# Optimization experiments

Hardware: AMD Instinct MI355X
Metric: run time of the kernel (lower is better)

Reference implementation:

```python
import jax, jax.numpy as jnp
import numpy as np

D_MODEL = 1024
N_HEADS = 16
H_DIM = D_MODEL // N_HEADS
B, T = 2, 2048


def setup_inputs() -> dict:
    key = jax.random.key(0)
    ks = jax.random.split(key, 11)
    s = 1.0 / np.sqrt(D_MODEL)
    inp = {
        "q": jax.random.normal(ks[0], (B, T, D_MODEL), dtype=jnp.float32),
        "k": jax.random.normal(ks[1], (B, T, D_MODEL), dtype=jnp.float32),
        "v": jax.random.normal(ks[2], (B, T, D_MODEL), dtype=jnp.float32),
        "Wq": jax.random.normal(ks[3], (D_MODEL, D_MODEL), dtype=jnp.float32) * s,
        "bq": jnp.zeros((D_MODEL,), dtype=jnp.float32),
        "Wk": jax.random.normal(ks[4], (D_MODEL, D_MODEL), dtype=jnp.float32) * s,
        "bk": jnp.zeros((D_MODEL,), dtype=jnp.float32),
        "Wv": jax.random.normal(ks[5], (D_MODEL, D_MODEL), dtype=jnp.float32) * s,
        "bv": jnp.zeros((D_MODEL,), dtype=jnp.float32),
        "Wo": jax.random.normal(ks[6], (D_MODEL, D_MODEL), dtype=jnp.float32) * s,
        "bo": jnp.zeros((D_MODEL,), dtype=jnp.float32),
    }
    return inp


def reference(q, k, v, Wq, bq, Wk, bk, Wv, bv, Wo, bo):
    # Linear projections (W stored so that y = x @ W + b)
    qp = q @ Wq + bq  # [B,T,D]
    kp = k @ Wk + bk
    vp = v @ Wv + bv
    Bz, Tz, _ = qp.shape
    # [B,T,H,h] -> [B,H,T,h]
    qh = qp.reshape(Bz, Tz, N_HEADS, H_DIM).transpose(0, 2, 1, 3)
    kh = kp.reshape(Bz, Tz, N_HEADS, H_DIM).transpose(0, 2, 1, 3)
    vh = vp.reshape(Bz, Tz, N_HEADS, H_DIM).transpose(0, 2, 1, 3)
    scale = 1.0 / np.sqrt(H_DIM).astype(np.float32)
    scores = jnp.einsum('bhqd,bhkd->bhqk', qh, kh) * scale  # [B,H,T,T]
    attn = jax.nn.softmax(scores, axis=-1)  # dropout is identity in eval
    ctx = jnp.einsum('bhqk,bhkd->bhqd', attn, vh)  # [B,H,T,h]
    ctx = ctx.transpose(0, 2, 1, 3).reshape(Bz, Tz, D_MODEL)
    return ctx @ Wo + bo
```

## Files before the change

### kernel.cpp

```cpp
#include <hip/hip_runtime.h>

typedef __bf16 bf16x8 __attribute__((ext_vector_type(8)));
typedef float f32x4 __attribute__((ext_vector_type(4)));
typedef float f32x16 __attribute__((ext_vector_type(16)));
typedef unsigned short u16;
typedef unsigned short u16x8 __attribute__((ext_vector_type(8)));
typedef unsigned int u32;

#define MROWS 4096
#define DMODEL 1024
#define TSEQ 2048

__device__ __forceinline__ u32 bfr(float x) {
    u32 u = __float_as_uint(x);
    return (u + 0x7FFFu + ((u >> 16) & 1u)) >> 16;
}
__device__ __forceinline__ u32 pk2(float lo, float hi) { return bfr(lo) | (bfr(hi) << 16); }

__device__ __forceinline__ u32 cvtpk(float lo, float hi) {
    u32 r;
    asm("v_cvt_pk_bf16_f32 %0, %1, %2" : "=v"(r) : "v"(lo), "v"(hi));
    return r;
}

__device__ __forceinline__ void gl_lds16(const void* g, void* l) {
    __builtin_amdgcn_global_load_lds(
        (const __attribute__((address_space(1))) unsigned int*)g,
        (__attribute__((address_space(3))) unsigned int*)l, 16, 0, 0);
}

__global__ __launch_bounds__(256) void cvt_x(const float* __restrict__ q,
                                             const float* __restrict__ k,
                                             const float* __restrict__ v,
                                             u16* __restrict__ X) {
    int z = blockIdx.y;
    const float* src = (z == 0) ? q : (z == 1) ? k : v;
    size_t idx = ((size_t)blockIdx.x * 256 + threadIdx.x) * 8;
    const float4* s4 = (const float4*)(src + idx);
    float4 a = s4[0], b = s4[1];
    uint4 r;
    r.x = pk2(a.x, a.y); r.y = pk2(a.z, a.w);
    r.z = pk2(b.x, b.y); r.w = pk2(b.z, b.w);
    *(uint4*)(X + (size_t)z * 4194304 + idx) = r;
}

__global__ __launch_bounds__(256) void cvt_w(const float* __restrict__ w0,
                                             const float* __restrict__ w1,
                                             const float* __restrict__ w2,
                                             const float* __restrict__ w3,
                                             u16* __restrict__ Wt) {
    int z = blockIdx.z;
    const float* W = (z == 0) ? w0 : (z == 1) ? w1 : (z == 2) ? w2 : w3;
    u16* dst = Wt + (size_t)z * 1048576;
    __shared__ float tile[32][33];
    int n0 = blockIdx.x * 32, k0 = blockIdx.y * 32;
    int tx = threadIdx.x & 31, ty = threadIdx.x >> 5;
#pragma unroll
    for (int r = 0; r < 4; r++) {
        int row = ty + r * 8;
        tile[row][tx] = W[(size_t)(k0 + row) * DMODEL + n0 + tx];
    }
    __syncthreads();
#pragma unroll
    for (int r = 0; r < 4; r++) {
        int row = ty + r * 8;
        dst[(size_t)(n0 + row) * DMODEL + k0 + tx] = (u16)bfr(tile[tx][row]);
    }
}

template <int OUT_BF16>
__global__ __launch_bounds__(256) void gemm_bt(const u16* __restrict__ Abase,
                                               const u16* __restrict__ Btbase,
                                               const float* __restrict__ b0,
                                               const float* __restrict__ b1,
                                               const float* __restrict__ b2,
                                               void* __restrict__ Cout, int ldc) {
    int z = blockIdx.z;
    const u16* A  = Abase + (size_t)z * MROWS * DMODEL;
    const u16* Bt = Btbase + (size_t)z * DMODEL * DMODEL;
    const float* bias = (z == 0) ? b0 : (z == 1) ? b1 : b2;
    int id = blockIdx.y * 8 + blockIdx.x;
    int swz = (id & 7) * 32 + (id >> 3);
    int brow = (swz >> 3) * 128, bcol = (swz & 7) * 128;
    int t = threadIdx.x, lane = t & 63, wid = t >> 6;
    int wr = wid >> 1, wc = wid & 1;
    int lrow = lane & 15, g = lane >> 4;

    __shared__ __align__(16) u16 Asm[2][128 * 32];
    __shared__ __align__(16) u16 Bsm[2][128 * 32];

    f32x4 zero4 = {0.f, 0.f, 0.f, 0.f};
    f32x4 acc[4][4];
#pragma unroll
    for (int i = 0; i < 4; i++)
#pragma unroll
        for (int j = 0; j < 4; j++) acc[i][j] = zero4;

    auto stage = [&](int buf, int kt) {
        int k0 = kt * 32;
#pragma unroll
        for (int i = 0; i < 2; i++) {
            int c = i * 256 + wid * 64 + lane;
            int row = c >> 2, kc = c & 3;
            gl_lds16(A + (size_t)(brow + row) * DMODEL + k0 + kc * 8,
                     &Asm[buf][(i * 256 + wid * 64) * 8]);
            gl_lds16(Bt + (size_t)(bcol + row) * DMODEL + k0 + kc * 8,
                     &Bsm[buf][(i * 256 + wid * 64) * 8]);
        }
    };

    stage(0, 0);
    __syncthreads();
    for (int kt = 0; kt < 32; ++kt) {
        int cur = kt & 1;
        if (kt < 31) stage(cur ^ 1, kt + 1);
        bf16x8 af[4], bfv[4];
#pragma unroll
        for (int mi = 0; mi < 4; mi++)
            af[mi] = *(const bf16x8*)&Asm[cur][(wr * 64 + mi * 16 + lrow) * 32 + g * 8];
#pragma unroll
        for (int nj = 0; nj < 4; nj++)
            bfv[nj] = *(const bf16x8*)&Bsm[cur][(wc * 64 + nj * 16 + lrow) * 32 + g * 8];
#pragma unroll
        for (int mi = 0; mi < 4; mi++)
#pragma unroll
            for (int nj = 0; nj < 4; nj++)
                acc[mi][nj] = __builtin_amdgcn_mfma_f32_16x16x32_bf16(af[mi], bfv[nj], acc[mi][nj], 0, 0, 0);
        __syncthreads();
    }
#pragma unroll
    for (int nj = 0; nj < 4; nj++) {
        int n = bcol + wc * 64 + nj * 16 + lrow;
        float bv = bias[n];
#pragma unroll
        for (int mi = 0; mi < 4; mi++) {
#pragma unroll
            for (int r = 0; r < 4; r++) {
                int row = brow + wr * 64 + mi * 16 + g * 4 + r;
                float val = acc[mi][nj][r] + bv;
                if (OUT_BF16)
                    ((u16*)Cout)[(size_t)row * ldc + z * DMODEL + n] = (u16)bfr(val);
                else
                    ((float*)Cout)[(size_t)row * ldc + n] = val;
            }
        }
    }
}

__global__ __launch_bounds__(512, 1) void attn(const u16* __restrict__ QKV, u16* __restrict__ CTX) {
    int id = blockIdx.y * 8 + blockIdx.x;
    int swz = (id & 7) * 32 + (id >> 3);
    int qt = swz & 7;
    int bh = swz >> 3;
    int head = bh & 15;
    size_t base = (size_t)(bh >> 4) * TSEQ * 3072;
    int t = threadIdx.x;
    int tl = t & 255;
    int grp = t >> 8;
    int lane = t & 63, wid = t >> 6;
    int lw = wid & 3;
    int l31 = lane & 31, hf = lane >> 5;

    __shared__ __align__(16) u16 SH[32768];
    u16* Kg = SH + grp * 16384;
    u16* Vg = SH + grp * 16384 + 8192;

    int qwave = qt * 256 + lw * 64;
    const u16* QpA = QKV + base + (size_t)(qwave + l31) * 3072 + head * 64;
    const u16* QpB = QpA + 32 * 3072;
    bf16x8 qfA[4], qfB[4];
#pragma unroll
    for (int c = 0; c < 4; c++) {
        qfA[c] = *(const bf16x8*)(QpA + c * 16 + hf * 8);
        qfB[c] = *(const bf16x8*)(QpB + c * 16 + hf * 8);
    }

    f32x16 oA0 = {}, oA1 = {}, oB0 = {}, oB1 = {};
    float lA = 0.f, lB = 0.f;
    const float mC = 0.18033688f;

    int vkv = (tl & 31) * 2;
    int vd0 = (tl >> 5) * 8;
    int vslot = (vkv & ~12) | ((vkv & 4) << 1) | ((vkv & 8) >> 1);
    u16x8 vr0, vr1;

    auto stageK = [&](int buf, int kvb) {
#pragma unroll
        for (int i = 0; i < 2; i++) {
            int c = i * 256 + lw * 64 + lane;
            int kv = c >> 3, kc = (c & 7) ^ (kv & 7);
            gl_lds16(QKV + base + (size_t)(kvb * 64 + kv) * 3072 + 1024 + head * 64 + kc * 8,
                     &Kg[buf * 4096 + (i * 256 + lw * 64) * 8]);
        }
    };
    auto loadV = [&](int kvb) {
        const u16* Vp = QKV + base + (size_t)(kvb * 64) * 3072 + 2048 + head * 64;
        vr0 = *(const u16x8*)(Vp + (size_t)vkv * 3072 + vd0);
        vr1 = *(const u16x8*)(Vp + (size_t)(vkv + 1) * 3072 + vd0);
    };
    auto writeV = [&](int buf) {
#pragma unroll
        for (int e = 0; e < 8; e++) {
            int d = vd0 + e;
            int kvs = vslot ^ ((d >> 4) << 4) ^ ((d & 7) << 3);
            u32 p = (u32)vr0[e] | ((u32)vr1[e] << 16);
            *(u32*)&Vg[buf * 4096 + d * 64 + kvs] = p;
        }
    };

    int kvb0 = grp * 16;
    stageK(0, kvb0);
    loadV(kvb0);
    writeV(0);
    __syncthreads();

    int kx = (l31 & 7) * 8;

    for (int j = 0; j < 16; ++j) {
        int cur = j & 1, nxt = cur ^ 1;
        if (j < 15) { stageK(nxt, kvb0 + j + 1); loadV(kvb0 + j + 1); }

        f32x16 s0A = {}, s1A = {}, s0B = {}, s1B = {};
        const u16* kr0 = &Kg[cur * 4096 + l31 * 64];
        const u16* kr1 = kr0 + 32 * 64;
        __builtin_amdgcn_s_setprio(1);
#pragma unroll
        for (int c = 0; c < 4; c++) {
            int slot = ((2 * c + hf) * 8) ^ kx;
            bf16x8 a0 = *(const bf16x8*)(kr0 + slot);
            bf16x8 a1 = *(const bf16x8*)(kr1 + slot);
            s0A = __builtin_amdgcn_mfma_f32_32x32x16_bf16(a0, qfA[c], s0A, 0, 0, 0);
            s1A = __builtin_amdgcn_mfma_f32_32x32x16_bf16(a1, qfA[c], s1A, 0, 0, 0);
            s0B = __builtin_amdgcn_mfma_f32_32x32x16_bf16(a0, qfB[c], s0B, 0, 0, 0);
            s1B = __builtin_amdgcn_mfma_f32_32x32x16_bf16(a1, qfB[c], s1B, 0, 0, 0);
        }
        __builtin_amdgcn_s_setprio(0);

        float p0A[16], p1A[16], p0B[16], p1B[16];
#pragma unroll
        for (int r = 0; r < 16; r++) {
            p0A[r] = __builtin_amdgcn_exp2f(s0A[r] * mC);
            p1A[r] = __builtin_amdgcn_exp2f(s1A[r] * mC);
            p0B[r] = __builtin_amdgcn_exp2f(s0B[r] * mC);
            p1B[r] = __builtin_amdgcn_exp2f(s1B[r] * mC);
        }
        float sa = 0.f, sb = 0.f, sc = 0.f, sd = 0.f;
#pragma unroll
        for (int r = 0; r < 8; r++) {
            sa += p0A[r] + p0A[r + 8];
            sb += p1A[r] + p1A[r + 8];
            sc += p0B[r] + p0B[r + 8];
            sd += p1B[r] + p1B[r + 8];
        }
        lA += sa + sb;
        lB += sc + sd;

        union FragU { u32 u[4]; bf16x8 v; };
        bf16x8 paA[4], paB[4];
        {
            FragU fA, fB2, fC, fD;
#pragma unroll
            for (int w = 0; w < 4; w++) {
                fA.u[w]  = cvtpk(p0A[2 * w],     p0A[2 * w + 1]);
                fB2.u[w] = cvtpk(p0A[8 + 2 * w], p0A[9 + 2 * w]);
                fC.u[w]  = cvtpk(p1A[2 * w],     p1A[2 * w + 1]);
                fD.u[w]  = cvtpk(p1A[8 + 2 * w], p1A[9 + 2 * w]);
            }
            paA[0] = fA.v; paA[1] = fB2.v; paA[2] = fC.v; paA[3] = fD.v;
#pragma unroll
            for (int w = 0; w < 4; w++) {
                fA.u[w]  = cvtpk(p0B[2 * w],     p0B[2 * w + 1]);
                fB2.u[w] = cvtpk(p0B[8 + 2 * w], p0B[9 + 2 * w]);
                fC.u[w]  = cvtpk(p1B[2 * w],     p1B[2 * w + 1]);
                fD.u[w]  = cvtpk(p1B[8 + 2 * w], p1B[9 + 2 * w]);
            }
            paB[0] = fA.v; paB[1] = fB2.v; paB[2] = fC.v; paB[3] = fD.v;
        }

        if (j < 15) writeV(nxt);

        __builtin_amdgcn_s_setprio(1);
#pragma unroll
        for (int kc = 0; kc < 4; kc++) {
            int d0 = l31;
            int sl0 = ((2 * kc + hf) ^ (d0 & 7) ^ ((d0 >> 4) << 1)) * 8;
            bf16x8 v0 = *(const bf16x8*)&Vg[cur * 4096 + d0 * 64 + sl0];
            int d1 = 32 + l31;
            int sl1 = ((2 * kc + hf) ^ (d1 & 7) ^ ((d1 >> 4) << 1)) * 8;
            bf16x8 v1 = *(const bf16x8*)&Vg[cur * 4096 + d1 * 64 + sl1];
            oA0 = __builtin_amdgcn_mfma_f32_32x32x16_bf16(paA[kc], v0, oA0, 0, 0, 0);
            oA1 = __builtin_amdgcn_mfma_f32_32x32x16_bf16(paA[kc], v1, oA1, 0, 0, 0);
            oB0 = __builtin_amdgcn_mfma_f32_32x32x16_bf16(paB[kc], v0, oB0, 0, 0, 0);
            oB1 = __builtin_amdgcn_mfma_f32_32x32x16_bf16(paB[kc], v1, oB1, 0, 0, 0);
        }
        __builtin_amdgcn_s_setprio(0);
        __syncthreads();
    }

    lA += __shfl_xor(lA, 32);
    lB += __shfl_xor(lB, 32);

    float* FB = (float*)SH;
    if (grp == 1) {
#pragma unroll
        for (int r = 0; r < 16; r++) {
            FB[lw * 2048 + r * 64 + lane]        = oA0[r];
            FB[lw * 2048 + 1024 + r * 64 + lane] = oA1[r];
        }
        FB[8192 + lw * 64 + lane] = lA;
    }
    __syncthreads();
    if (grp == 0) {
        float l1 = FB[8192 + lw * 64 + lane];
        float rl = 1.0f / (lA + l1);
#pragma unroll
        for (int r = 0; r < 16; r++) {
            int qr = (r & 3) + 8 * (r >> 2) + 4 * hf;
            float rr = __shfl(rl, qr);
            float po0 = FB[lw * 2048 + r * 64 + lane];
            float po1 = FB[lw * 2048 + 1024 + r * 64 + lane];
            size_t rowoff = ((size_t)(bh >> 4) * TSEQ + qwave + qr) * DMODEL + head * 64;
            CTX[rowoff + l31]      = (u16)bfr((oA0[r] + po0) * rr);
            CTX[rowoff + 32 + l31] = (u16)bfr((oA1[r] + po1) * rr);
        }
    }
    __syncthreads();
    if (grp == 1) {
#pragma unroll
        for (int r = 0; r < 16; r++) {
            FB[lw * 2048 + r * 64 + lane]        = oB0[r];
            FB[lw * 2048 + 1024 + r * 64 + lane] = oB1[r];
        }
        FB[8192 + lw * 64 + lane] = lB;
    }
    __syncthreads();
    if (grp == 0) {
        float l1 = FB[8192 + lw * 64 + lane];
        float rl = 1.0f / (lB + l1);
#pragma unroll
        for (int r = 0; r < 16; r++) {
            int qr = (r & 3) + 8 * (r >> 2) + 4 * hf;
            float rr = __shfl(rl, qr);
            float po0 = FB[lw * 2048 + r * 64 + lane];
            float po1 = FB[lw * 2048 + 1024 + r * 64 + lane];
            size_t rowoff = ((size_t)(bh >> 4) * TSEQ + qwave + 32 + qr) * DMODEL + head * 64;
            CTX[rowoff + l31]      = (u16)bfr((oB0[r] + po0) * rr);
            CTX[rowoff + 32 + l31] = (u16)bfr((oB1[r] + po1) * rr);
        }
    }
}

extern "C" void kernel_launch(void* const* d_in, const int* in_sizes, int n_in,
                              void* d_out, int out_size, void* d_ws, size_t ws_size,
                              hipStream_t stream) {
    const float* q  = (const float*)d_in[0];
    const float* k  = (const float*)d_in[1];
    const float* v  = (const float*)d_in[2];
    const float* Wq = (const float*)d_in[3];
    const float* bq = (const float*)d_in[4];
    const float* Wk = (const float*)d_in[5];
    const float* bk = (const float*)d_in[6];
    const float* Wv = (const float*)d_in[7];
    const float* bv = (const float*)d_in[8];
    const float* Wo = (const float*)d_in[9];
    const float* bo = (const float*)d_in[10];

    char* ws = (char*)d_ws;
    u16* Xbf = (u16*)ws;
    u16* Wt  = (u16*)(ws + 25165824);
    u16* QKV = (u16*)(ws + 25165824 + 8388608);
    u16* CTX = Xbf;

    cvt_x<<<dim3(2048, 3), 256, 0, stream>>>(q, k, v, Xbf);
    cvt_w<<<dim3(32, 32, 4), 256, 0, stream>>>(Wq, Wk, Wv, Wo, Wt);
    gemm_bt<1><<<dim3(8, 32, 3), 256, 0, stream>>>(Xbf, Wt, bq, bk, bv, QKV, 3072);
    attn<<<dim3(8, 32), 512, 0, stream>>>(QKV, CTX);
    gemm_bt<0><<<dim3(8, 32, 1), 256, 0, stream>>>(CTX, Wt + 3 * 1048576, bo, bo, bo, d_out, 1024);
}
```

Measured before the change: 125.7 us.

## Fuse fp32-to-bf16 input conversion into QKV GEMM and split attention KV four ways

Drops the separate cvt_x kernel: the QKV projection GEMM now reads fp32 activations directly into registers, converts them to bf16 with v_cvt_pk_bf16_f32 and writes them to LDS. This removes one kernel launch and a full bf16 round trip of the activations through HBM, but A loads are now register-staged rather than direct-to-LDS. Separately, the attention kernel moves to 1024 threads with four KV-split groups of 8 blocks each, single-buffered K/V and an extra barrier per iteration. Partial outputs are combined across four groups through LDS in four phases, which raises parallelism but adds synchronization and reduction cost.

```diff
diff --git a/kernel.cpp b/kernel.cpp
--- a/kernel.cpp
+++ b/kernel.cpp
@@ -15,7 +15,6 @@
     u32 u = __float_as_uint(x);
     return (u + 0x7FFFu + ((u >> 16) & 1u)) >> 16;
 }
-__device__ __forceinline__ u32 pk2(float lo, float hi) { return bfr(lo) | (bfr(hi) << 16); }
 
 __device__ __forceinline__ u32 cvtpk(float lo, float hi) {
     u32 r;
@@ -27,21 +26,6 @@
     __builtin_amdgcn_global_load_lds(
         (const __attribute__((address_space(1))) unsigned int*)g,
         (__attribute__((address_space(3))) unsigned int*)l, 16, 0, 0);
-}
-
-__global__ __launch_bounds__(256) void cvt_x(const float* __restrict__ q,
-                                             const float* __restrict__ k,
-                                             const float* __restrict__ v,
-                                             u16* __restrict__ X) {
-    int z = blockIdx.y;
-    const float* src = (z == 0) ? q : (z == 1) ? k : v;
-    size_t idx = ((size_t)blockIdx.x * 256 + threadIdx.x) * 8;
-    const float4* s4 = (const float4*)(src + idx);
-    float4 a = s4[0], b = s4[1];
-    uint4 r;
-    r.x = pk2(a.x, a.y); r.y = pk2(a.z, a.w);
-    r.z = pk2(b.x, b.y); r.w = pk2(b.z, b.w);
-    *(uint4*)(X + (size_t)z * 4194304 + idx) = r;
 }
 
 __global__ __launch_bounds__(256) void cvt_w(const float* __restrict__ w0,
@@ -68,15 +52,17 @@
     }
 }
 
-template <int OUT_BF16>
-__global__ __launch_bounds__(256) void gemm_bt(const u16* __restrict__ Abase,
+template <int A_F32, int OUT_BF16>
+__global__ __launch_bounds__(256) void gemm_bt(const void* __restrict__ a0,
+                                               const void* __restrict__ a1,
+                                               const void* __restrict__ a2,
                                                const u16* __restrict__ Btbase,
                                                const float* __restrict__ b0,
                                                const float* __restrict__ b1,
                                                const float* __restrict__ b2,
                                                void* __restrict__ Cout, int ldc) {
     int z = blockIdx.z;
-    const u16* A  = Abase + (size_t)z * MROWS * DMODEL;
+    const void* Az = (z == 0) ? a0 : (z == 1) ? a1 : a2;
     const u16* Bt = Btbase + (size_t)z * DMODEL * DMODEL;
     const float* bias = (z == 0) ? b0 : (z == 1) ? b1 : b2;
     int id = blockIdx.y * 8 + blockIdx.x;
@@ -96,24 +82,63 @@
 #pragma unroll
         for (int j = 0; j < 4; j++) acc[i][j] = zero4;
 
-    auto stage = [&](int buf, int kt) {
+    float4 ar[2][2];
+
+    auto issueA = [&](int kt) {
         int k0 = kt * 32;
 #pragma unroll
         for (int i = 0; i < 2; i++) {
             int c = i * 256 + wid * 64 + lane;
             int row = c >> 2, kc = c & 3;
-            gl_lds16(A + (size_t)(brow + row) * DMODEL + k0 + kc * 8,
+            const float* ap = (const float*)Az + (size_t)(brow + row) * DMODEL + k0 + kc * 8;
+            ar[i][0] = *(const float4*)ap;
+            ar[i][1] = *(const float4*)(ap + 4);
+        }
+    };
+    auto writeA = [&](int buf) {
+#pragma unroll
+        for (int i = 0; i < 2; i++) {
+            int c = i * 256 + wid * 64 + lane;
+            uint4 w;
+            w.x = cvtpk(ar[i][0].x, ar[i][0].y);
+            w.y = cvtpk(ar[i][0].z, ar[i][0].w);
+            w.z = cvtpk(ar[i][1].x, ar[i][1].y);
+            w.w = cvtpk(ar[i][1].z, ar[i][1].w);
+            *(uint4*)&Asm[buf][c * 8] = w;
+        }
+    };
+    auto stageA16 = [&](int buf, int kt) {
+        int k0 = kt * 32;
+#pragma unroll
+        for (int i = 0; i < 2; i++) {
+            int c = i * 256 + wid * 64 + lane;
+            int row = c >> 2, kc = c & 3;
+            gl_lds16((const u16*)Az + (size_t)(brow + row) * DMODEL + k0 + kc * 8,
                      &Asm[buf][(i * 256 + wid * 64) * 8]);
+        }
+    };
+    auto stageB = [&](int buf, int kt) {
+        int k0 = kt * 32;
+#pragma unroll
+        for (int i = 0; i < 2; i++) {
+            int c = i * 256 + wid * 64 + lane;
+            int row = c >> 2, kc = c & 3;
             gl_lds16(Bt + (size_t)(bcol + row) * DMODEL + k0 + kc * 8,
                      &Bsm[buf][(i * 256 + wid * 64) * 8]);
         }
     };
 
-    stage(0, 0);
-    __syncthreads();
+    if constexpr (A_F32) { issueA(0); stageB(0, 0); writeA(0); }
+    else                 { stageA16(0, 0); stageB(0, 0); }
+    __syncthreads();
+
     for (int kt = 0; kt < 32; ++kt) {
-        int cur = kt & 1;
-        if (kt < 31) stage(cur ^ 1, kt + 1);
+        int cur = kt & 1, nxt = cur ^ 1;
+        if (kt < 31) {
+            if constexpr (A_F32) issueA(kt + 1);
+            else                 stageA16(nxt, kt + 1);
+            stageB(nxt, kt + 1);
+        }
         bf16x8 af[4], bfv[4];
 #pragma unroll
         for (int mi = 0; mi < 4; mi++)
@@ -126,6 +151,7 @@
 #pragma unroll
             for (int nj = 0; nj < 4; nj++)
                 acc[mi][nj] = __builtin_amdgcn_mfma_f32_16x16x32_bf16(af[mi], bfv[nj], acc[mi][nj], 0, 0, 0);
+        if constexpr (A_F32) { if (kt < 31) writeA(nxt); }
         __syncthreads();
     }
 #pragma unroll
@@ -147,7 +173,7 @@
     }
 }
 
-__global__ __launch_bounds__(512, 1) void attn(const u16* __restrict__ QKV, u16* __restrict__ CTX) {
+__global__ __launch_bounds__(1024, 1) void attn(const u16* __restrict__ QKV, u16* __restrict__ CTX) {
     int id = blockIdx.y * 8 + blockIdx.x;
     int swz = (id & 7) * 32 + (id >> 3);
     int qt = swz & 7;
@@ -157,13 +183,13 @@
     int t = threadIdx.x;
     int tl = t & 255;
     int grp = t >> 8;
-    int lane = t & 63, wid = t >> 6;
-    int lw = wid & 3;
+    int lane = t & 63;
+    int lw = (t >> 6) & 3;
     int l31 = lane & 31, hf = lane >> 5;
 
     __shared__ __align__(16) u16 SH[32768];
-    u16* Kg = SH + grp * 16384;
-    u16* Vg = SH + grp * 16384 + 8192;
+    u16* Kl = SH + grp * 8192;
+    u16* Vl = SH + grp * 8192 + 4096;
 
     int qwave = qt * 256 + lw * 64;
     const u16* QpA = QKV + base + (size_t)(qwave + l31) * 3072 + head * 64;
@@ -184,13 +210,13 @@
     int vslot = (vkv & ~12) | ((vkv & 4) << 1) | ((vkv & 8) >> 1);
     u16x8 vr0, vr1;
 
-    auto stageK = [&](int buf, int kvb) {
+    auto stageK = [&](int kvb) {
 #pragma unroll
         for (int i = 0; i < 2; i++) {
             int c = i * 256 + lw * 64 + lane;
             int kv = c >> 3, kc = (c & 7) ^ (kv & 7);
             gl_lds16(QKV + base + (size_t)(kvb * 64 + kv) * 3072 + 1024 + head * 64 + kc * 8,
-                     &Kg[buf * 4096 + (i * 256 + lw * 64) * 8]);
+                     &Kl[(i * 256 + lw * 64) * 8]);
         }
     };
     auto loadV = [&](int kvb) {
@@ -198,30 +224,28 @@
         vr0 = *(const u16x8*)(Vp + (size_t)vkv * 3072 + vd0);
         vr1 = *(const u16x8*)(Vp + (size_t)(vkv + 1) * 3072 + vd0);
     };
-    auto writeV = [&](int buf) {
+    auto writeV = [&]() {
 #pragma unroll
         for (int e = 0; e < 8; e++) {
             int d = vd0 + e;
             int kvs = vslot ^ ((d >> 4) << 4) ^ ((d & 7) << 3);
             u32 p = (u32)vr0[e] | ((u32)vr1[e] << 16);
-            *(u32*)&Vg[buf * 4096 + d * 64 + kvs] = p;
-        }
-    };
-
-    int kvb0 = grp * 16;
-    stageK(0, kvb0);
+            *(u32*)&Vl[d * 64 + kvs] = p;
+        }
+    };
+
+    int kvb0 = grp * 8;
     loadV(kvb0);
-    writeV(0);
+    stageK(kvb0);
     __syncthreads();
 
     int kx = (l31 & 7) * 8;
 
-    for (int j = 0; j < 16; ++j) {
-        int cur = j & 1, nxt = cur ^ 1;
-        if (j < 15) { stageK(nxt, kvb0 + j + 1); loadV(kvb0 + j + 1); }
+    for (int j = 0; j < 8; ++j) {
+        writeV();
 
         f32x16 s0A = {}, s1A = {}, s0B = {}, s1B = {};
-        const u16* kr0 = &Kg[cur * 4096 + l31 * 64];
+        const u16* kr0 = &Kl[l31 * 64];
         const u16* kr1 = kr0 + 32 * 64;
         __builtin_amdgcn_s_setprio(1);
 #pragma unroll
@@ -236,6 +260,8 @@
         }
         __builtin_amdgcn_s_setprio(0);
 
+        if (j < 7) loadV(kvb0 + j + 1);
+
         float p0A[16], p1A[16], p0B[16], p1B[16];
 #pragma unroll
         for (int r = 0; r < 16; r++) {
@@ -277,17 +303,19 @@
             paB[0] = fA.v; paB[1] = fB2.v; paB[2] = fC.v; paB[3] = fD.v;
         }
 
-        if (j < 15) writeV(nxt);
+        __syncthreads();
+
+        if (j < 7) stageK(kvb0 + j + 1);
 
         __builtin_amdgcn_s_setprio(1);
 #pragma unroll
         for (int kc = 0; kc < 4; kc++) {
             int d0 = l31;
             int sl0 = ((2 * kc + hf) ^ (d0 & 7) ^ ((d0 >> 4) << 1)) * 8;
-            bf16x8 v0 = *(const bf16x8*)&Vg[cur * 4096 + d0 * 64 + sl0];
+            bf16x8 v0 = *(const bf16x8*)&Vl[d0 * 64 + sl0];
             int d1 = 32 + l31;
             int sl1 = ((2 * kc + hf) ^ (d1 & 7) ^ ((d1 >> 4) << 1)) * 8;
-            bf16x8 v1 = *(const bf16x8*)&Vg[cur * 4096 + d1 * 64 + sl1];
+            bf16x8 v1 = *(const bf16x8*)&Vl[d1 * 64 + sl1];
             oA0 = __builtin_amdgcn_mfma_f32_32x32x16_bf16(paA[kc], v0, oA0, 0, 0, 0);
             oA1 = __builtin_amdgcn_mfma_f32_32x32x16_bf16(paA[kc], v1, oA1, 0, 0, 0);
             oB0 = __builtin_amdgcn_mfma_f32_32x32x16_bf16(paB[kc], v0, oB0, 0, 0, 0);
@@ -301,51 +329,88 @@
     lB += __shfl_xor(lB, 32);
 
     float* FB = (float*)SH;
-    if (grp == 1) {
-#pragma unroll
-        for (int r = 0; r < 16; r++) {
-            FB[lw * 2048 + r * 64 + lane]        = oA0[r];
-            FB[lw * 2048 + 1024 + r * 64 + lane] = oA1[r];
-        }
-        FB[8192 + lw * 64 + lane] = lA;
-    }
-    __syncthreads();
-    if (grp == 0) {
-        float l1 = FB[8192 + lw * 64 + lane];
-        float rl = 1.0f / (lA + l1);
+    int slot = (grp - 1) * 4 + lw;
+    float rlA = 0.f, rlB = 0.f;
+
+    if (grp) {
+#pragma unroll
+        for (int r = 0; r < 16; r++) FB[slot * 1024 + r * 64 + lane] = oA0[r];
+        FB[12288 + slot * 64 + lane] = lA;
+    }
+    __syncthreads();
+    if (!grp) {
+        float ltot = lA;
+#pragma unroll
+        for (int g2 = 0; g2 < 3; g2++) ltot += FB[12288 + (g2 * 4 + lw) * 64 + lane];
+        rlA = 1.0f / ltot;
 #pragma unroll
         for (int r = 0; r < 16; r++) {
             int qr = (r & 3) + 8 * (r >> 2) + 4 * hf;
-            float rr = __shfl(rl, qr);
-            float po0 = FB[lw * 2048 + r * 64 + lane];
-            float po1 = FB[lw * 2048 + 1024 + r * 64 + lane];
+            float rr = __shfl(rlA, qr);
+            float sum = oA0[r];
+#pragma unroll
+            for (int g2 = 0; g2 < 3; g2++) sum += FB[(g2 * 4 + lw) * 1024 + r * 64 + lane];
             size_t rowoff = ((size_t)(bh >> 4) * TSEQ + qwave + qr) * DMODEL + head * 64;
-            CTX[rowoff + l31]      = (u16)bfr((oA0[r] + po0) * rr);
-            CTX[rowoff + 32 + l31] = (u16)bfr((oA1[r] + po1) * rr);
-        }
-    }
-    __syncthreads();
-    if (grp == 1) {
-#pragma unroll
-        for (int r = 0; r < 16; r++) {
-            FB[lw * 2048 + r * 64 + lane]        = oB0[r];
-            FB[lw * 2048 + 1024 + r * 64 + lane] = oB1[r];
-        }
-        FB[8192 + lw * 64 + lane] = lB;
-    }
-    __syncthreads();
-    if (grp == 0) {
-        float l1 = FB[8192 + lw * 64 + lane];
-        float rl = 1.0f / (lB + l1);
+            CTX[rowoff + l31] = (u16)bfr(sum * rr);
+        }
+    }
+    __syncthreads();
+    if (grp) {
+#pragma unroll
+        for (int r = 0; r < 16; r++) FB[slot * 1024 + r * 64 + lane] = oA1[r];
+    }
+    __syncthreads();
+    if (!grp) {
 #pragma unroll
         for (int r = 0; r < 16; r++) {
             int qr = (r & 3) + 8 * (r >> 2) + 4 * hf;
-            float rr = __shfl(rl, qr);
-            float po0 = FB[lw * 2048 + r * 64 + lane];
-            float po1 = FB[lw * 2048 + 1024 + r * 64 + lane];
+            float rr = __shfl(rlA, qr);
+            float sum = oA1[r];
+#pragma unroll
+            for (int g2 = 0; g2 < 3; g2++) sum += FB[(g2 * 4 + lw) * 1024 + r * 64 + lane];
+            size_t rowoff = ((size_t)(bh >> 4) * TSEQ + qwave + qr) * DMODEL + head * 64;
+            CTX[rowoff + 32 + l31] = (u16)bfr(sum * rr);
+        }
+    }
+    __syncthreads();
+    if (grp) {
+#pragma unroll
+        for (int r = 0; r < 16; r++) FB[slot * 1024 + r * 64 + lane] = oB0[r];
+        FB[12288 + slot * 64 + lane] = lB;
+    }
+    __syncthreads();
+    if (!grp) {
+        float ltot = lB;
+#pragma unroll
+        for (int g2 = 0; g2 < 3; g2++) ltot += FB[12288 + (g2 * 4 + lw) * 64 + lane];
+        rlB = 1.0f / ltot;
+#pragma unroll
+        for (int r = 0; r < 16; r++) {
+            int qr = (r & 3) + 8 * (r >> 2) + 4 * hf;
+            float rr = __shfl(rlB, qr);
+            float sum = oB0[r];
+#pragma unroll
+            for (int g2 = 0; g2 < 3; g2++) sum += FB[(g2 * 4 + lw) * 1024 + r * 64 + lane];
             size_t rowoff = ((size_t)(bh >> 4) * TSEQ + qwave + 32 + qr) * DMODEL + head * 64;
-            CTX[rowoff + l31]      = (u16)bfr((oB0[r] + po0) * rr);
-            CTX[rowoff + 32 + l31] = (u16)bfr((oB1[r] + po1) * rr);
+            CTX[rowoff + l31] = (u16)bfr(sum * rr);
+        }
+    }
+    __syncthreads();
+    if (grp) {
+#pragma unroll
+        for (int r = 0; r < 16; r++) FB[slot * 1024 + r * 64 + lane] = oB1[r];
+    }
+    __syncthreads();
+    if (!grp) {
+#pragma unroll
+        for (int r = 0; r < 16; r++) {
+            int qr = (r & 3) + 8 * (r >> 2) + 4 * hf;
+            float rr = __shfl(rlB, qr);
+            float sum = oB1[r];
+#pragma unroll
+            for (int g2 = 0; g2 < 3; g2++) sum += FB[(g2 * 4 + lw) * 1024 + r * 64 + lane];
+            size_t rowoff = ((size_t)(bh >> 4) * TSEQ + qwave + 32 + qr) * DMODEL + head * 64;
+            CTX[rowoff + 32 + l31] = (u16)bfr(sum * rr);
         }
     }
 }
@@ -366,14 +431,12 @@
     const float* bo = (const float*)d_in[10];
 
     char* ws = (char*)d_ws;
-    u16* Xbf = (u16*)ws;
+    u16* CTX = (u16*)ws;
     u16* Wt  = (u16*)(ws + 25165824);
     u16* QKV = (u16*)(ws + 25165824 + 8388608);
-    u16* CTX = Xbf;
-
-    cvt_x<<<dim3(2048, 3), 256, 0, stream>>>(q, k, v, Xbf);
+
     cvt_w<<<dim3(32, 32, 4), 256, 0, stream>>>(Wq, Wk, Wv, Wo, Wt);
-    gemm_bt<1><<<dim3(8, 32, 3), 256, 0, stream>>>(Xbf, Wt, bq, bk, bv, QKV, 3072);
-    attn<<<dim3(8, 32), 512, 0, stream>>>(QKV, CTX);
-    gemm_bt<0><<<dim3(8, 32, 1), 256, 0, stream>>>(CTX, Wt + 3 * 1048576, bo, bo, bo, d_out, 1024);
-}
+    gemm_bt<1, 1><<<dim3(8, 32, 3), 256, 0, stream>>>(q, k, v, Wt, bq, bk, bv, QKV, 3072);
+    attn<<<dim3(8, 32), 1024, 0, stream>>>(QKV, CTX);
+    gemm_bt<0, 0><<<dim3(8, 32, 1), 256, 0, stream>>>(CTX, CTX, CTX, Wt + 3 * 1048576, bo, bo, bo, d_out, 1024);
+}
```

Result: slower. 334.6 us (+166.1%).
